# Kernel optimization log

Measured on AMD Instinct MI355X. Metric: run time of the kernel, lower is better.

The kernel has to match this reference:

```python
import math
import jax, jax.numpy as jnp
import numpy as np

H = 64  # lstm_hidden_size
T = 9   # seq_len


def _lstm_layer(pre, w_hh):
    """pre: [N, T, 4H] = x @ W_ih^T + b_ih + b_hh; w_hh: [4H, H].
    Returns full hidden sequence [N, T, H]. Gate order (PyTorch): i, f, g, o."""
    N = pre.shape[0]
    pre_t = jnp.transpose(pre, (1, 0, 2))  # [T, N, 4H]
    h0 = jnp.zeros((N, H), dtype=pre.dtype)
    c0 = jnp.zeros((N, H), dtype=pre.dtype)

    def step(carry, xt):
        h, c = carry
        g = xt + h @ w_hh.T  # [N, 4H]
        i = jax.nn.sigmoid(g[:, 0 * H:1 * H])
        f = jax.nn.sigmoid(g[:, 1 * H:2 * H])
        gg = jnp.tanh(g[:, 2 * H:3 * H])
        o = jax.nn.sigmoid(g[:, 3 * H:4 * H])
        c = f * c + i * gg
        h = o * jnp.tanh(c)
        return (h, c), h

    _, hs = jax.lax.scan(step, (h0, c0), pre_t)  # hs: [T, N, H]
    return jnp.transpose(hs, (1, 0, 2))  # [N, T, H]


def _forward(xy, w_ih0, w_hh0, b0, w_ih1, w_hh1, b1,
             fus_w, fus_b, res_w1, res_b1, res_w2, res_b2,
             head_w1, head_b1, head_w2, head_b2):
    x = xy[:, 0:1]
    y = xy[:, 1:2]
    pi = math.pi
    # seq: [N, 9, 1]
    seq = jnp.stack([x, y, x ** 2, y ** 2, x * y,
                     jnp.sin(pi * x), jnp.cos(pi * x),
                     jnp.sin(pi * y), jnp.cos(pi * y)], axis=1)
    # layer 0: input size 1
    pre0 = jnp.einsum('ntd,gd->ntg', seq, w_ih0) + b0  # [N, T, 4H]
    h_seq0 = _lstm_layer(pre0, w_hh0)                   # [N, T, H]
    # layer 1: input size H
    pre1 = jnp.einsum('nth,gh->ntg', h_seq0, w_ih1) + b1
    h_seq1 = _lstm_layer(pre1, w_hh1)
    feat = h_seq1[:, -1, :]                             # [N, H]

    fused = jnp.concatenate([feat, xy], axis=1)         # [N, H+2]
    z = jnp.tanh(fused @ fus_w.T + fus_b)               # [N, 64]
    for k in range(res_w1.shape[0]):
        t = jnp.tanh(z @ res_w1[k].T + res_b1[k])
        z = z + jnp.tanh(t @ res_w2[k].T + res_b2[k])
    h = jnp.tanh(z @ head_w1.T + head_b1)
    return h @ head_w2.T + head_b2                      # [N, 5]


def setup_inputs() -> dict:
    key = jax.random.key(0)
    ks = jax.random.split(key, 20)
    N = 262144
    D = 64  # fc_hidden_dim
    xy = jax.random.uniform(ks[0], (N, 2), dtype=jnp.float32)

    def w(k, shape, scale=0.1):
        return (jax.random.normal(k, shape, dtype=jnp.float32) * scale)

    inp = {
        'xy': xy,
        'w_ih0': w(ks[1], (4 * H, 1)),
        'w_hh0': w(ks[2], (4 * H, H)),
        'b0': jnp.zeros((4 * H,), jnp.float32),
        'w_ih1': w(ks[3], (4 * H, H)),
        'w_hh1': w(ks[4], (4 * H, H)),
        'b1': jnp.zeros((4 * H,), jnp.float32),
        'fus_w': w(ks[5], (D, H + 2)),
        'fus_b': jnp.zeros((D,), jnp.float32),
        'res_w1': w(ks[6], (3, D, D)),
        'res_b1': jnp.zeros((3, D), jnp.float32),
        'res_w2': w(ks[7], (3, D, D)),
        'res_b2': jnp.zeros((3, D), jnp.float32),
        'head_w1': w(ks[8], (D, D)),
        'head_b1': jnp.zeros((D,), jnp.float32),
        'head_w2': w(ks[9], (5, D)),
        'head_b2': jnp.zeros((5,), jnp.float32),
    }
    return inp


def reference(xy, w_ih0, w_hh0, b0, w_ih1, w_hh1, b1,
              fus_w, fus_b, res_w1, res_b1, res_w2, res_b2,
              head_w1, head_b1, head_w2, head_b2):
    return _forward(xy, w_ih0, w_hh0, b0, w_ih1, w_hh1, b1,
                    fus_w, fus_b, res_w1, res_b1, res_w2, res_b2,
                    head_w1, head_b1, head_w2, head_b2)
```

## Files before the change

kernel.cpp:

```cpp
#include <hip/hip_runtime.h>
#include <math.h>

#define PI_F 3.14159265358979323846f
#define WAVES 15
#define TPB (WAVES*64)
#define TPB2 512

#define GS_IFO (-1.4426950408889634f)
#define GS_G   (-2.8853900817779268f)

typedef _Float16 half_t;
typedef __attribute__((ext_vector_type(8))) _Float16 f16x8;
typedef __attribute__((ext_vector_type(4))) float f32x4;

union F16x8U { f16x8 v; unsigned int u[4]; half_t h[8]; };

__device__ __forceinline__ float frcp(float x)  { return __builtin_amdgcn_rcpf(x); }
__device__ __forceinline__ float fexp2(float x) { return __builtin_amdgcn_exp2f(x); }
__device__ __forceinline__ float ftanh(float x) { return 1.0f - 2.0f * frcp(1.0f + __expf(2.0f * x)); }

__device__ __forceinline__ float2 lstm_gate(float ai, float af, float ag, float ao, float cold) {
    float ui = fexp2(ai);
    float uf = fexp2(af);
    float ug = fexp2(ag);
    float uo = fexp2(ao);
    float ig = (1.0f - ug) * frcp((1.0f + ui) * (1.0f + ug));
    float ff = frcp(1.0f + uf);
    float cv = fmaf(ff, cold, ig);
    float uc = fexp2(GS_G * cv);
    float hh = (1.0f - uc) * frcp((1.0f + uo) * (1.0f + uc));
    return make_float2(cv, hh);
}

#define MFMA16(a,b,c) __builtin_amdgcn_mfma_f32_16x16x32_f16((a),(b),(c),0,0,0)

#define AUG_B   98304
#define B1_B    99328
#define EPI_H   50176
#define BIAS_B  172032
#define HOUT_H  88064
#define EF_FUS  0
#define EF_R1   6144
#define EF_R2   18432
#define EF_HW1  30720
#define EF_HW2  34816

__global__ void pack_weights(const float* __restrict__ w_ih0, const float* __restrict__ w_hh0, const float* __restrict__ b0,
                             const float* __restrict__ w_ih1, const float* __restrict__ w_hh1, const float* __restrict__ b1,
                             const float* __restrict__ fus_w, const float* __restrict__ fus_b,
                             const float* __restrict__ res_w1, const float* __restrict__ res_b1,
                             const float* __restrict__ res_w2, const float* __restrict__ res_b2,
                             const float* __restrict__ head_w1, const float* __restrict__ head_b1,
                             const float* __restrict__ head_w2, const float* __restrict__ head_b2,
                             half_t* __restrict__ hws)
{
    int id = blockIdx.x * blockDim.x + threadIdx.x;

    if (id < 6144) {
        int ln = id & 63, rest = id >> 6;
        int kb = rest & 1, cb = (rest >> 1) & 15, mat = rest >> 5;
        const float* W = (mat == 0) ? w_hh0 : ((mat == 1) ? w_ih1 : w_hh1);
        const int gate = cb >> 2;
        const float sc = (gate == 2) ? GS_G : GS_IFO;
        const float* src = W + (cb * 16 + (ln & 15)) * 64 + kb * 32 + (ln >> 4) * 8;
        F16x8U t;
        #pragma unroll
        for (int i = 0; i < 8; ++i) t.h[i] = (half_t)(sc * src[i]);
        *(f16x8*)&hws[id * 8] = t.v;
        return;
    }
    id -= 6144;
    if (id < 256) {
        const int gate = id >> 6;
        const float sc = (gate == 2) ? GS_G : GS_IFO;
        F16x8U t; t.u[0] = 0;
        t.h[0] = (half_t)(sc * w_ih0[id]);
        t.h[1] = (half_t)(sc * b0[id]);
        ((unsigned int*)((char*)hws + AUG_B))[id] = t.u[0];
        return;
    }
    id -= 256;
    if (id < 256) {
        const int gate = id >> 6;
        const float sc = (gate == 2) ? GS_G : GS_IFO;
        ((float*)((char*)hws + B1_B))[id] = sc * b1[id];
        return;
    }
    id -= 256;
    if (id < 768) {
        int ln = id & 63, rest = id >> 6;
        int kb = rest % 3, cb = rest / 3;
        int col = cb * 16 + (ln & 15), q = ln >> 4;
        F16x8U t; t.u[0] = t.u[1] = t.u[2] = t.u[3] = 0;
        if (kb < 2) {
            #pragma unroll
            for (int i = 0; i < 8; ++i) t.h[i] = (half_t)fus_w[col * 66 + kb * 32 + q * 8 + i];
        } else if (q == 0) {
            t.h[0] = (half_t)fus_w[col * 66 + 64];
            t.h[1] = (half_t)fus_w[col * 66 + 65];
            t.h[2] = (half_t)fus_b[col];
        }
        *(f16x8*)&hws[(EPI_H + EF_FUS + id * 8)] = t.v;
        return;
    }
    id -= 768;
    if (id < 1536) {
        int ln = id & 63, rest = id >> 6;
        int kb = rest & 1, cb = (rest >> 1) & 3, rb = rest >> 3;
        int col = cb * 16 + (ln & 15), q = ln >> 4;
        F16x8U t;
        #pragma unroll
        for (int i = 0; i < 8; ++i) t.h[i] = (half_t)res_w1[rb * 4096 + col * 64 + kb * 32 + q * 8 + i];
        *(f16x8*)&hws[(EPI_H + EF_R1 + id * 8)] = t.v;
        return;
    }
    id -= 1536;
    if (id < 1536) {
        int ln = id & 63, rest = id >> 6;
        int kb = rest & 1, cb = (rest >> 1) & 3, rb = rest >> 3;
        int col = cb * 16 + (ln & 15), q = ln >> 4;
        F16x8U t;
        #pragma unroll
        for (int i = 0; i < 8; ++i) t.h[i] = (half_t)res_w2[rb * 4096 + col * 64 + kb * 32 + q * 8 + i];
        *(f16x8*)&hws[(EPI_H + EF_R2 + id * 8)] = t.v;
        return;
    }
    id -= 1536;
    if (id < 512) {
        int ln = id & 63, rest = id >> 6;
        int kb = rest & 1, cb = rest >> 1;
        int col = cb * 16 + (ln & 15), q = ln >> 4;
        F16x8U t;
        #pragma unroll
        for (int i = 0; i < 8; ++i) t.h[i] = (half_t)head_w1[col * 64 + kb * 32 + q * 8 + i];
        *(f16x8*)&hws[(EPI_H + EF_HW1 + id * 8)] = t.v;
        return;
    }
    id -= 512;
    if (id < 128) {
        int ln = id & 63, kb = id >> 6;
        int col = ln & 15, q = ln >> 4;
        F16x8U t; t.u[0] = t.u[1] = t.u[2] = t.u[3] = 0;
        if (col < 5) {
            #pragma unroll
            for (int i = 0; i < 8; ++i) t.h[i] = (half_t)head_w2[col * 64 + kb * 32 + q * 8 + i];
        }
        *(f16x8*)&hws[(EPI_H + EF_HW2 + id * 8)] = t.v;
        return;
    }
    id -= 128;
    if (id < 517) {
        float v;
        if      (id < 64)  v = fus_b[id];
        else if (id < 256) v = res_b1[id - 64];
        else if (id < 448) v = res_b2[id - 256];
        else if (id < 512) v = head_b1[id - 448];
        else               v = head_b2[id - 512];
        ((float*)((char*)hws + BIAS_B))[id] = v;
        return;
    }
}

__global__ __launch_bounds__(TPB, 2)
void lstm_core(const float* __restrict__ xy, const half_t* __restrict__ hws, int N)
{
    __shared__ __align__(16) half_t wlds[3][16][2][64][8];
    __shared__ __align__(16) half_t hfrag[WAVES][2][2][64][8];
    __shared__ unsigned int aug_lds[256];
    __shared__ float b1_lds[256];

    const int lane = threadIdx.x & 63;
    const int wid  = threadIdx.x >> 6;
    const int cc   = lane & 15;
    const int qq   = lane >> 4;

    for (int idx = threadIdx.x; idx < 6144; idx += TPB)
        *(f16x8*)&((half_t*)wlds)[idx * 8] = *(const f16x8*)&hws[idx * 8];
    if (threadIdx.x < 256) {
        aug_lds[threadIdx.x] = ((const unsigned int*)((const char*)hws + AUG_B))[threadIdx.x];
        b1_lds[threadIdx.x]  = ((const float*)((const char*)hws + B1_B))[threadIdx.x];
    }
    __syncthreads();

    const int tile = blockIdx.x * WAVES + wid;
    const int S = tile * 16;
    if (S >= N) return;

    int si = S + cc; if (si >= N) si = N - 1;
    const float fx = xy[2 * si + 0];
    const float fy = xy[2 * si + 1];
    float feat[9];
    feat[0] = fx; feat[1] = fy; feat[2] = fx * fx; feat[3] = fy * fy; feat[4] = fx * fy;
    feat[5] = sinf(PI_F * fx); feat[6] = cosf(PI_F * fx);
    feat[7] = sinf(PI_F * fy); feat[8] = cosf(PI_F * fy);

    {
        F16x8U Z; Z.u[0] = Z.u[1] = Z.u[2] = Z.u[3] = 0;
        *(f16x8*)&hfrag[wid][0][0][lane][0] = Z.v;
        *(f16x8*)&hfrag[wid][0][1][lane][0] = Z.v;
        *(f16x8*)&hfrag[wid][1][0][lane][0] = Z.v;
        *(f16x8*)&hfrag[wid][1][1][lane][0] = Z.v;
    }
    float c0s[4][4], c1s[4][4];
    #pragma unroll
    for (int a = 0; a < 4; ++a)
        #pragma unroll
        for (int b = 0; b < 4; ++b) { c0s[a][b] = 0.0f; c1s[a][b] = 0.0f; }

    asm volatile("" ::: "memory");

    #pragma unroll 1
    for (int t = 0; t < 9; ++t) {
        float ftv;
        switch (t) {
            case 0: ftv = feat[0]; break;  case 1: ftv = feat[1]; break;
            case 2: ftv = feat[2]; break;  case 3: ftv = feat[3]; break;
            case 4: ftv = feat[4]; break;  case 5: ftv = feat[5]; break;
            case 6: ftv = feat[6]; break;  case 7: ftv = feat[7]; break;
            default: ftv = feat[8]; break;
        }
        F16x8U AG; AG.u[0] = AG.u[1] = AG.u[2] = AG.u[3] = 0;
        if (qq == 0) { AG.h[0] = (half_t)ftv; AG.h[1] = (half_t)1.0f; }

        f16x8 a00 = *(const f16x8*)&hfrag[wid][0][0][lane][0];
        f16x8 a01 = *(const f16x8*)&hfrag[wid][0][1][lane][0];
        #pragma unroll
        for (int jj = 0; jj < 4; ++jj) {
            f32x4 acc[4];
            #pragma unroll
            for (int g = 0; g < 4; ++g) {
                const int cb = jj + 4 * g;
                F16x8U BA; BA.u[0] = (qq == 0) ? aug_lds[cb * 16 + cc] : 0u;
                BA.u[1] = 0; BA.u[2] = 0; BA.u[3] = 0;
                f32x4 a = {0.f, 0.f, 0.f, 0.f};
                a = MFMA16(AG.v, BA.v, a);
                f16x8 bf0 = *(const f16x8*)&wlds[0][cb][0][lane][0];
                f16x8 bf1 = *(const f16x8*)&wlds[0][cb][1][lane][0];
                a = MFMA16(a00, bf0, a);
                a = MFMA16(a01, bf1, a);
                acc[g] = a;
            }
            const int kb = jj >> 1;
            half_t* hp = &hfrag[wid][0][kb][0][0];
            const int lb = (4 * qq + 16 * ((2 * jj + (cc >> 3)) & 3)) * 8 + (cc & 7);
            #pragma unroll
            for (int r = 0; r < 4; ++r) {
                float2 ch = lstm_gate(acc[0][r], acc[1][r], acc[2][r], acc[3][r], c0s[jj][r]);
                c0s[jj][r] = ch.x;
                hp[lb + 8 * r] = (half_t)ch.y;
            }
        }
        asm volatile("" ::: "memory");

        f16x8 a10 = *(const f16x8*)&hfrag[wid][0][0][lane][0];
        f16x8 a11 = *(const f16x8*)&hfrag[wid][0][1][lane][0];
        f16x8 a12 = *(const f16x8*)&hfrag[wid][1][0][lane][0];
        f16x8 a13 = *(const f16x8*)&hfrag[wid][1][1][lane][0];
        #pragma unroll
        for (int jj = 0; jj < 4; ++jj) {
            f32x4 acc[4];
            #pragma unroll
            for (int g = 0; g < 4; ++g) {
                const int cb = jj + 4 * g;
                const float bv = b1_lds[cb * 16 + cc];
                f32x4 a = {bv, bv, bv, bv};
                f16x8 bi0 = *(const f16x8*)&wlds[1][cb][0][lane][0];
                f16x8 bi1 = *(const f16x8*)&wlds[1][cb][1][lane][0];
                f16x8 bh0 = *(const f16x8*)&wlds[2][cb][0][lane][0];
                f16x8 bh1 = *(const f16x8*)&wlds[2][cb][1][lane][0];
                a = MFMA16(a10, bi0, a);
                a = MFMA16(a11, bi1, a);
                a = MFMA16(a12, bh0, a);
                a = MFMA16(a13, bh1, a);
                acc[g] = a;
            }
            const int kb = jj >> 1;
            half_t* hp = &hfrag[wid][1][kb][0][0];
            const int lb = (4 * qq + 16 * ((2 * jj + (cc >> 3)) & 3)) * 8 + (cc & 7);
            #pragma unroll
            for (int r = 0; r < 4; ++r) {
                float2 ch = lstm_gate(acc[0][r], acc[1][r], acc[2][r], acc[3][r], c1s[jj][r]);
                c1s[jj][r] = ch.x;
                hp[lb + 8 * r] = (half_t)ch.y;
            }
        }
        asm volatile("" ::: "memory");
    }

    half_t* hout = (half_t*)hws + HOUT_H + (size_t)tile * 1024;
    *(f16x8*)&hout[0   + lane * 8] = *(const f16x8*)&hfrag[wid][1][0][lane][0];
    *(f16x8*)&hout[512 + lane * 8] = *(const f16x8*)&hfrag[wid][1][1][lane][0];
}

__global__ __launch_bounds__(TPB2, 1)
void epi_mlp(const float* __restrict__ xy, const half_t* __restrict__ hws,
             float* __restrict__ out, int ntiles, int N)
{
    __shared__ __align__(16) half_t ef[35840];
    __shared__ float biasl[517];
    __shared__ __align__(16) half_t hbuf[8][2][2][64][8];

    for (int idx = threadIdx.x; idx < 4480; idx += TPB2)
        *(f16x8*)&ef[idx * 8] = *(const f16x8*)&hws[(EPI_H + idx * 8)];
    const float* bg = (const float*)((const char*)hws + BIAS_B);
    for (int i = threadIdx.x; i < 517; i += TPB2) biasl[i] = bg[i];
    __syncthreads();

    const half_t* hout = hws + HOUT_H;
    const int lane = threadIdx.x & 63;
    const int wid  = threadIdx.x >> 6;
    const int cc   = lane & 15;
    const int qq   = lane >> 4;
    const int gw = blockIdx.x * 8 + wid;
    const int nw = gridDim.x * 8;

#define WRITE_ACT(BUF, VALS) do {                                              \
        _Pragma("unroll")                                                      \
        for (int cb = 0; cb < 4; ++cb) {                                       \
            half_t* hp = &hbuf[wid][BUF][cb >> 1][0][0];                       \
            const int lb = (4*qq + 16*((2*cb + (cc>>3)) & 3))*8 + (cc & 7);    \
            _Pragma("unroll")                                                  \
            for (int r = 0; r < 4; ++r) hp[lb + 8*r] = (half_t)(VALS)[cb][r];  \
        }                                                                      \
        asm volatile("" ::: "memory");                                         \
    } while (0)

    #pragma unroll 1
    for (int tile = gw; tile < ntiles; tile += nw) {
        const size_t hob = (size_t)tile * 1024;
        f16x8 e0 = *(const f16x8*)&hout[hob + lane * 8];
        f16x8 e1 = *(const f16x8*)&hout[hob + 512 + lane * 8];

        int s = tile * 16 + cc; if (s >= N) s = N - 1;
        const float fx = xy[2 * s], fy = xy[2 * s + 1];
        F16x8U AF; AF.u[0] = AF.u[1] = AF.u[2] = AF.u[3] = 0;
        if (qq == 0) { AF.h[0] = (half_t)fx; AF.h[1] = (half_t)fy; AF.h[2] = (half_t)1.0f; }

        float zz[4][4];
        #pragma unroll
        for (int cb = 0; cb < 4; ++cb) {
            f32x4 a = {0.f, 0.f, 0.f, 0.f};
            a = MFMA16(e0,   *(const f16x8*)&ef[(EF_FUS + ((cb * 3 + 0) * 64 + lane) * 8)], a);
            a = MFMA16(e1,   *(const f16x8*)&ef[(EF_FUS + ((cb * 3 + 1) * 64 + lane) * 8)], a);
            a = MFMA16(AF.v, *(const f16x8*)&ef[(EF_FUS + ((cb * 3 + 2) * 64 + lane) * 8)], a);
            #pragma unroll
            for (int r = 0; r < 4; ++r) zz[cb][r] = ftanh(a[r]);
        }
        WRITE_ACT(0, zz);
        f16x8 za0 = *(const f16x8*)&hbuf[wid][0][0][lane][0];
        f16x8 za1 = *(const f16x8*)&hbuf[wid][0][1][lane][0];

        #pragma unroll 1
        for (int rb = 0; rb < 3; ++rb) {
            float tt[4][4];
            #pragma unroll
            for (int cb = 0; cb < 4; ++cb) {
                const float bv = biasl[64 + rb * 64 + cb * 16 + cc];
                f32x4 a = {bv, bv, bv, bv};
                a = MFMA16(za0, *(const f16x8*)&ef[(EF_R1 + (((rb * 4 + cb) * 2 + 0) * 64 + lane) * 8)], a);
                a = MFMA16(za1, *(const f16x8*)&ef[(EF_R1 + (((rb * 4 + cb) * 2 + 1) * 64 + lane) * 8)], a);
                #pragma unroll
                for (int r = 0; r < 4; ++r) tt[cb][r] = ftanh(a[r]);
            }
            WRITE_ACT(1, tt);
            f16x8 ta0 = *(const f16x8*)&hbuf[wid][1][0][lane][0];
            f16x8 ta1 = *(const f16x8*)&hbuf[wid][1][1][lane][0];
            #pragma unroll
            for (int cb = 0; cb < 4; ++cb) {
                const float bv = biasl[256 + rb * 64 + cb * 16 + cc];
                f32x4 a = {bv, bv, bv, bv};
                a = MFMA16(ta0, *(const f16x8*)&ef[(EF_R2 + (((rb * 4 + cb) * 2 + 0) * 64 + lane) * 8)], a);
                a = MFMA16(ta1, *(const f16x8*)&ef[(EF_R2 + (((rb * 4 + cb) * 2 + 1) * 64 + lane) * 8)], a);
                #pragma unroll
                for (int r = 0; r < 4; ++r) zz[cb][r] += ftanh(a[r]);
            }
            WRITE_ACT(0, zz);
            za0 = *(const f16x8*)&hbuf[wid][0][0][lane][0];
            za1 = *(const f16x8*)&hbuf[wid][0][1][lane][0];
        }

        float hh[4][4];
        #pragma unroll
        for (int cb = 0; cb < 4; ++cb) {
            const float bv = biasl[448 + cb * 16 + cc];
            f32x4 a = {bv, bv, bv, bv};
            a = MFMA16(za0, *(const f16x8*)&ef[(EF_HW1 + ((cb * 2 + 0) * 64 + lane) * 8)], a);
            a = MFMA16(za1, *(const f16x8*)&ef[(EF_HW1 + ((cb * 2 + 1) * 64 + lane) * 8)], a);
            #pragma unroll
            for (int r = 0; r < 4; ++r) hh[cb][r] = ftanh(a[r]);
        }
        WRITE_ACT(1, hh);
        f16x8 ha0 = *(const f16x8*)&hbuf[wid][1][0][lane][0];
        f16x8 ha1 = *(const f16x8*)&hbuf[wid][1][1][lane][0];

        {
            const float bv = (cc < 5) ? biasl[512 + cc] : 0.0f;
            f32x4 a = {bv, bv, bv, bv};
            a = MFMA16(ha0, *(const f16x8*)&ef[(EF_HW2 + ((0) * 64 + lane) * 8)], a);
            a = MFMA16(ha1, *(const f16x8*)&ef[(EF_HW2 + ((1) * 64 + lane) * 8)], a);
            if (cc < 5) {
                #pragma unroll
                for (int r = 0; r < 4; ++r) {
                    const int row = tile * 16 + 4 * qq + r;
                    if (row < N) out[row * 5 + cc] = a[r];
                }
            }
        }
    }
#undef WRITE_ACT
}

extern "C" void kernel_launch(void* const* d_in, const int* in_sizes, int n_in,
                              void* d_out, int out_size, void* d_ws, size_t ws_size,
                              hipStream_t stream) {
    const float* xy      = (const float*)d_in[0];
    const float* w_ih0   = (const float*)d_in[1];
    const float* w_hh0   = (const float*)d_in[2];
    const float* b0      = (const float*)d_in[3];
    const float* w_ih1   = (const float*)d_in[4];
    const float* w_hh1   = (const float*)d_in[5];
    const float* b1      = (const float*)d_in[6];
    const float* fus_w   = (const float*)d_in[7];
    const float* fus_b   = (const float*)d_in[8];
    const float* res_w1  = (const float*)d_in[9];
    const float* res_b1  = (const float*)d_in[10];
    const float* res_w2  = (const float*)d_in[11];
    const float* res_b2  = (const float*)d_in[12];
    const float* head_w1 = (const float*)d_in[13];
    const float* head_b1 = (const float*)d_in[14];
    const float* head_w2 = (const float*)d_in[15];
    const float* head_b2 = (const float*)d_in[16];

    const int N = in_sizes[0] / 2;
    const int ntiles = (N + 15) / 16;
    half_t* hws = (half_t*)d_ws;

    pack_weights<<<dim3(46), dim3(256), 0, stream>>>(
        w_ih0, w_hh0, b0, w_ih1, w_hh1, b1,
        fus_w, fus_b, res_w1, res_b1, res_w2, res_b2,
        head_w1, head_b1, head_w2, head_b2, hws);

    const int grid1 = (ntiles + WAVES - 1) / WAVES;
    lstm_core<<<dim3(grid1), dim3(TPB), 0, stream>>>(xy, hws, N);

    epi_mlp<<<dim3(256), dim3(TPB2), 0, stream>>>(xy, hws, (float*)d_out, ntiles, N);
}
```

Before: 514.0 us.

## Process two 16-row tiles per wave in LSTM core to reuse weight fragments

Each wave now runs two independent 16-sample tiles through both LSTM layers, so every weight fragment read from LDS feeds two MFMA chains. The two chains also give independent work to interleave and hide MFMA and transcendental latency. The augmented input weights and layer-1 bias move from LDS into per-lane registers, and waves per block drop from 15 to 8. The cost is higher register pressure from doubled accumulators and cell state, which may lower occupancy.

Result: faster. 457.2 us (median of 2 runs) (-11.0%).

```diff
diff --git a/kernel.cpp b/kernel.cpp
--- a/kernel.cpp
+++ b/kernel.cpp
@@ -2,7 +2,7 @@
 #include <math.h>
 
 #define PI_F 3.14159265358979323846f
-#define WAVES 15
+#define WAVES 8
 #define TPB (WAVES*64)
 #define TPB2 512
 
@@ -165,9 +165,7 @@
 void lstm_core(const float* __restrict__ xy, const half_t* __restrict__ hws, int N)
 {
     __shared__ __align__(16) half_t wlds[3][16][2][64][8];
-    __shared__ __align__(16) half_t hfrag[WAVES][2][2][64][8];
-    __shared__ unsigned int aug_lds[256];
-    __shared__ float b1_lds[256];
+    __shared__ __align__(16) half_t hfrag[WAVES][2][2][2][64][8];
 
     const int lane = threadIdx.x & 63;
     const int wid  = threadIdx.x >> 6;
@@ -176,120 +174,179 @@
 
     for (int idx = threadIdx.x; idx < 6144; idx += TPB)
         *(f16x8*)&((half_t*)wlds)[idx * 8] = *(const f16x8*)&hws[idx * 8];
-    if (threadIdx.x < 256) {
-        aug_lds[threadIdx.x] = ((const unsigned int*)((const char*)hws + AUG_B))[threadIdx.x];
-        b1_lds[threadIdx.x]  = ((const float*)((const char*)hws + B1_B))[threadIdx.x];
-    }
     __syncthreads();
 
-    const int tile = blockIdx.x * WAVES + wid;
-    const int S = tile * 16;
-    if (S >= N) return;
-
-    int si = S + cc; if (si >= N) si = N - 1;
-    const float fx = xy[2 * si + 0];
-    const float fy = xy[2 * si + 1];
-    float feat[9];
-    feat[0] = fx; feat[1] = fy; feat[2] = fx * fx; feat[3] = fy * fy; feat[4] = fx * fy;
-    feat[5] = sinf(PI_F * fx); feat[6] = cosf(PI_F * fx);
-    feat[7] = sinf(PI_F * fy); feat[8] = cosf(PI_F * fy);
+    unsigned int augr[16];
+    float b1r[16];
+    {
+        const unsigned int* at = (const unsigned int*)((const char*)hws + AUG_B);
+        const float* bt = (const float*)((const char*)hws + B1_B);
+        #pragma unroll
+        for (int cb = 0; cb < 16; ++cb) {
+            augr[cb] = (qq == 0) ? at[cb * 16 + cc] : 0u;
+            b1r[cb]  = bt[cb * 16 + cc];
+        }
+    }
+
+    const int pair = blockIdx.x * WAVES + wid;
+    const int S0 = pair * 32;
+    if (S0 >= N) return;
+
+    int si0 = S0 + cc;      if (si0 >= N) si0 = N - 1;
+    int si1 = S0 + 16 + cc; if (si1 >= N) si1 = N - 1;
+    const float fx0 = xy[2 * si0], fy0 = xy[2 * si0 + 1];
+    const float fx1 = xy[2 * si1], fy1 = xy[2 * si1 + 1];
+    float feat0[9], feat1[9];
+    feat0[0] = fx0; feat0[1] = fy0; feat0[2] = fx0 * fx0; feat0[3] = fy0 * fy0; feat0[4] = fx0 * fy0;
+    feat0[5] = sinf(PI_F * fx0); feat0[6] = cosf(PI_F * fx0);
+    feat0[7] = sinf(PI_F * fy0); feat0[8] = cosf(PI_F * fy0);
+    feat1[0] = fx1; feat1[1] = fy1; feat1[2] = fx1 * fx1; feat1[3] = fy1 * fy1; feat1[4] = fx1 * fy1;
+    feat1[5] = sinf(PI_F * fx1); feat1[6] = cosf(PI_F * fx1);
+    feat1[7] = sinf(PI_F * fy1); feat1[8] = cosf(PI_F * fy1);
 
     {
         F16x8U Z; Z.u[0] = Z.u[1] = Z.u[2] = Z.u[3] = 0;
-        *(f16x8*)&hfrag[wid][0][0][lane][0] = Z.v;
-        *(f16x8*)&hfrag[wid][0][1][lane][0] = Z.v;
-        *(f16x8*)&hfrag[wid][1][0][lane][0] = Z.v;
-        *(f16x8*)&hfrag[wid][1][1][lane][0] = Z.v;
-    }
-    float c0s[4][4], c1s[4][4];
+        #pragma unroll
+        for (int p = 0; p < 2; ++p)
+            #pragma unroll
+            for (int b = 0; b < 2; ++b)
+                #pragma unroll
+                for (int kb = 0; kb < 2; ++kb)
+                    *(f16x8*)&hfrag[wid][p][b][kb][lane][0] = Z.v;
+    }
+    float c0s[2][4][4], c1s[2][4][4];
     #pragma unroll
-    for (int a = 0; a < 4; ++a)
-        #pragma unroll
-        for (int b = 0; b < 4; ++b) { c0s[a][b] = 0.0f; c1s[a][b] = 0.0f; }
+    for (int p = 0; p < 2; ++p)
+        #pragma unroll
+        for (int a = 0; a < 4; ++a)
+            #pragma unroll
+            for (int b = 0; b < 4; ++b) { c0s[p][a][b] = 0.0f; c1s[p][a][b] = 0.0f; }
 
     asm volatile("" ::: "memory");
 
     #pragma unroll 1
     for (int t = 0; t < 9; ++t) {
-        float ftv;
+        float ftv0, ftv1;
         switch (t) {
-            case 0: ftv = feat[0]; break;  case 1: ftv = feat[1]; break;
-            case 2: ftv = feat[2]; break;  case 3: ftv = feat[3]; break;
-            case 4: ftv = feat[4]; break;  case 5: ftv = feat[5]; break;
-            case 6: ftv = feat[6]; break;  case 7: ftv = feat[7]; break;
-            default: ftv = feat[8]; break;
-        }
-        F16x8U AG; AG.u[0] = AG.u[1] = AG.u[2] = AG.u[3] = 0;
-        if (qq == 0) { AG.h[0] = (half_t)ftv; AG.h[1] = (half_t)1.0f; }
-
-        f16x8 a00 = *(const f16x8*)&hfrag[wid][0][0][lane][0];
-        f16x8 a01 = *(const f16x8*)&hfrag[wid][0][1][lane][0];
+            case 0: ftv0 = feat0[0]; ftv1 = feat1[0]; break;
+            case 1: ftv0 = feat0[1]; ftv1 = feat1[1]; break;
+            case 2: ftv0 = feat0[2]; ftv1 = feat1[2]; break;
+            case 3: ftv0 = feat0[3]; ftv1 = feat1[3]; break;
+            case 4: ftv0 = feat0[4]; ftv1 = feat1[4]; break;
+            case 5: ftv0 = feat0[5]; ftv1 = feat1[5]; break;
+            case 6: ftv0 = feat0[6]; ftv1 = feat1[6]; break;
+            case 7: ftv0 = feat0[7]; ftv1 = feat1[7]; break;
+            default: ftv0 = feat0[8]; ftv1 = feat1[8]; break;
+        }
+        F16x8U AG0, AG1;
+        AG0.u[0] = AG0.u[1] = AG0.u[2] = AG0.u[3] = 0;
+        AG1.u[0] = AG1.u[1] = AG1.u[2] = AG1.u[3] = 0;
+        if (qq == 0) {
+            AG0.h[0] = (half_t)ftv0; AG0.h[1] = (half_t)1.0f;
+            AG1.h[0] = (half_t)ftv1; AG1.h[1] = (half_t)1.0f;
+        }
+
+        f16x8 p0a0 = *(const f16x8*)&hfrag[wid][0][0][0][lane][0];
+        f16x8 p0a1 = *(const f16x8*)&hfrag[wid][0][0][1][lane][0];
+        f16x8 p1a0 = *(const f16x8*)&hfrag[wid][1][0][0][lane][0];
+        f16x8 p1a1 = *(const f16x8*)&hfrag[wid][1][0][1][lane][0];
         #pragma unroll
         for (int jj = 0; jj < 4; ++jj) {
-            f32x4 acc[4];
+            f32x4 acc0[4], acc1[4];
             #pragma unroll
             for (int g = 0; g < 4; ++g) {
                 const int cb = jj + 4 * g;
-                F16x8U BA; BA.u[0] = (qq == 0) ? aug_lds[cb * 16 + cc] : 0u;
-                BA.u[1] = 0; BA.u[2] = 0; BA.u[3] = 0;
-                f32x4 a = {0.f, 0.f, 0.f, 0.f};
-                a = MFMA16(AG.v, BA.v, a);
+                F16x8U BA; BA.u[0] = augr[cb]; BA.u[1] = 0; BA.u[2] = 0; BA.u[3] = 0;
                 f16x8 bf0 = *(const f16x8*)&wlds[0][cb][0][lane][0];
                 f16x8 bf1 = *(const f16x8*)&wlds[0][cb][1][lane][0];
-                a = MFMA16(a00, bf0, a);
-                a = MFMA16(a01, bf1, a);
-                acc[g] = a;
+                f32x4 a0 = {0.f, 0.f, 0.f, 0.f};
+                a0 = MFMA16(AG0.v, BA.v, a0);
+                a0 = MFMA16(p0a0, bf0, a0);
+                a0 = MFMA16(p0a1, bf1, a0);
+                acc0[g] = a0;
+                f32x4 a1 = {0.f, 0.f, 0.f, 0.f};
+                a1 = MFMA16(AG1.v, BA.v, a1);
+                a1 = MFMA16(p1a0, bf0, a1);
+                a1 = MFMA16(p1a1, bf1, a1);
+                acc1[g] = a1;
             }
             const int kb = jj >> 1;
-            half_t* hp = &hfrag[wid][0][kb][0][0];
             const int lb = (4 * qq + 16 * ((2 * jj + (cc >> 3)) & 3)) * 8 + (cc & 7);
+            half_t* hp0 = &hfrag[wid][0][0][kb][0][0];
+            half_t* hp1 = &hfrag[wid][1][0][kb][0][0];
             #pragma unroll
             for (int r = 0; r < 4; ++r) {
-                float2 ch = lstm_gate(acc[0][r], acc[1][r], acc[2][r], acc[3][r], c0s[jj][r]);
-                c0s[jj][r] = ch.x;
-                hp[lb + 8 * r] = (half_t)ch.y;
+                float2 ch0 = lstm_gate(acc0[0][r], acc0[1][r], acc0[2][r], acc0[3][r], c0s[0][jj][r]);
+                c0s[0][jj][r] = ch0.x;
+                hp0[lb + 8 * r] = (half_t)ch0.y;
+                float2 ch1 = lstm_gate(acc1[0][r], acc1[1][r], acc1[2][r], acc1[3][r], c0s[1][jj][r]);
+                c0s[1][jj][r] = ch1.x;
+                hp1[lb + 8 * r] = (half_t)ch1.y;
             }
         }
         asm volatile("" ::: "memory");
 
-        f16x8 a10 = *(const f16x8*)&hfrag[wid][0][0][lane][0];
-        f16x8 a11 = *(const f16x8*)&hfrag[wid][0][1][lane][0];
-        f16x8 a12 = *(const f16x8*)&hfrag[wid][1][0][lane][0];
-        f16x8 a13 = *(const f16x8*)&hfrag[wid][1][1][lane][0];
+        f16x8 q0a0 = *(const f16x8*)&hfrag[wid][0][0][0][lane][0];
+        f16x8 q0a1 = *(const f16x8*)&hfrag[wid][0][0][1][lane][0];
+        f16x8 q0b0 = *(const f16x8*)&hfrag[wid][0][1][0][lane][0];
+        f16x8 q0b1 = *(const f16x8*)&hfrag[wid][0][1][1][lane][0];
+        f16x8 q1a0 = *(const f16x8*)&hfrag[wid][1][0][0][lane][0];
+        f16x8 q1a1 = *(const f16x8*)&hfrag[wid][1][0][1][lane][0];
+        f16x8 q1b0 = *(const f16x8*)&hfrag[wid][1][1][0][lane][0];
+        f16x8 q1b1 = *(const f16x8*)&hfrag[wid][1][1][1][lane][0];
         #pragma unroll
         for (int jj = 0; jj < 4; ++jj) {
-            f32x4 acc[4];
+            f32x4 acc0[4], acc1[4];
             #pragma unroll
             for (int g = 0; g < 4; ++g) {
                 const int cb = jj + 4 * g;
-                const float bv = b1_lds[cb * 16 + cc];
-                f32x4 a = {bv, bv, bv, bv};
+                const float bv = b1r[cb];
                 f16x8 bi0 = *(const f16x8*)&wlds[1][cb][0][lane][0];
                 f16x8 bi1 = *(const f16x8*)&wlds[1][cb][1][lane][0];
                 f16x8 bh0 = *(const f16x8*)&wlds[2][cb][0][lane][0];
                 f16x8 bh1 = *(const f16x8*)&wlds[2][cb][1][lane][0];
-                a = MFMA16(a10, bi0, a);
-                a = MFMA16(a11, bi1, a);
-                a = MFMA16(a12, bh0, a);
-                a = MFMA16(a13, bh1, a);
-                acc[g] = a;
+                f32x4 a0 = {bv, bv, bv, bv};
+                a0 = MFMA16(q0a0, bi0, a0);
+                a0 = MFMA16(q0a1, bi1, a0);
+                a0 = MFMA16(q0b0, bh0, a0);
+                a0 = MFMA16(q0b1, bh1, a0);
+                acc0[g] = a0;
+                f32x4 a1 = {bv, bv, bv, bv};
+                a1 = MFMA16(q1a0, bi0, a1);
+                a1 = MFMA16(q1a1, bi1, a1);
+                a1 = MFMA16(q1b0, bh0, a1);
+                a1 = MFMA16(q1b1, bh1, a1);
+                acc1[g] = a1;
             }
             const int kb = jj >> 1;
-            half_t* hp = &hfrag[wid][1][kb][0][0];
             const int lb = (4 * qq + 16 * ((2 * jj + (cc >> 3)) & 3)) * 8 + (cc & 7);
+            half_t* hp0 = &hfrag[wid][0][1][kb][0][0];
+            half_t* hp1 = &hfrag[wid][1][1][kb][0][0];
             #pragma unroll
             for (int r = 0; r < 4; ++r) {
-                float2 ch = lstm_gate(acc[0][r], acc[1][r], acc[2][r], acc[3][r], c1s[jj][r]);
-                c1s[jj][r] = ch.x;
-                hp[lb + 8 * r] = (half_t)ch.y;
+                float2 ch0 = lstm_gate(acc0[0][r], acc0[1][r], acc0[2][r], acc0[3][r], c1s[0][jj][r]);
+                c1s[0][jj][r] = ch0.x;
+                hp0[lb + 8 * r] = (half_t)ch0.y;
+                float2 ch1 = lstm_gate(acc1[0][r], acc1[1][r], acc1[2][r], acc1[3][r], c1s[1][jj][r]);
+                c1s[1][jj][r] = ch1.x;
+                hp1[lb + 8 * r] = (half_t)ch1.y;
             }
         }
         asm volatile("" ::: "memory");
     }
 
-    half_t* hout = (half_t*)hws + HOUT_H + (size_t)tile * 1024;
-    *(f16x8*)&hout[0   + lane * 8] = *(const f16x8*)&hfrag[wid][1][0][lane][0];
-    *(f16x8*)&hout[512 + lane * 8] = *(const f16x8*)&hfrag[wid][1][1][lane][0];
+    const int ntiles = (N + 15) >> 4;
+    {
+        const int tile0 = pair * 2;
+        half_t* hout = (half_t*)hws + HOUT_H + (size_t)tile0 * 1024;
+        *(f16x8*)&hout[0   + lane * 8] = *(const f16x8*)&hfrag[wid][0][1][0][lane][0];
+        *(f16x8*)&hout[512 + lane * 8] = *(const f16x8*)&hfrag[wid][0][1][1][lane][0];
+        if (tile0 + 1 < ntiles) {
+            half_t* hout1 = (half_t*)hws + HOUT_H + (size_t)(tile0 + 1) * 1024;
+            *(f16x8*)&hout1[0   + lane * 8] = *(const f16x8*)&hfrag[wid][1][1][0][lane][0];
+            *(f16x8*)&hout1[512 + lane * 8] = *(const f16x8*)&hfrag[wid][1][1][1][lane][0];
+        }
+    }
 }
 
 __global__ __launch_bounds__(TPB2, 1)
@@ -433,6 +490,7 @@
 
     const int N = in_sizes[0] / 2;
     const int ntiles = (N + 15) / 16;
+    const int npairs = (ntiles + 1) / 2;
     half_t* hws = (half_t*)d_ws;
 
     pack_weights<<<dim3(46), dim3(256), 0, stream>>>(
@@ -440,7 +498,7 @@
         fus_w, fus_b, res_w1, res_b1, res_w2, res_b2,
         head_w1, head_b1, head_w2, head_b2, hws);
 
-    const int grid1 = (ntiles + WAVES - 1) / WAVES;
+    const int grid1 = (npairs + WAVES - 1) / WAVES;
     lstm_core<<<dim3(grid1), dim3(TPB), 0, stream>>>(xy, hws, N);
 
     epi_mlp<<<dim3(256), dim3(TPB2), 0, stream>>>(xy, hws, (float*)d_out, ntiles, N);
```
